# Kernel tuning notes

Hardware: AMD Instinct MI355X
Metric: run time of the kernel (lower is better)

Reference implementation:

```python
import math
import jax, jax.numpy as jnp
import numpy as np

D_MODEL = 1024
N_HEADS = 16
HEAD_DIM = D_MODEL // N_HEADS
D_FF = 4096
LN_EPS = 1e-5


def _layer_norm(x, g, b):
    mu = jnp.mean(x, axis=-1, keepdims=True)
    var = jnp.var(x, axis=-1, keepdims=True)
    return (x - mu) * jax.lax.rsqrt(var + LN_EPS) * g + b


def setup_inputs() -> dict:
    key = jax.random.key(0)
    ks = jax.random.split(key, 8)
    s = 0.02
    d, dff = D_MODEL, D_FF
    return {
        "src": jax.random.normal(ks[0], (2, 2048, d), dtype=jnp.float32),
        "in_proj_w": jax.random.normal(ks[1], (3 * d, d), dtype=jnp.float32) * s,
        "in_proj_b": jnp.zeros((3 * d,), dtype=jnp.float32),
        "out_w": jax.random.normal(ks[2], (d, d), dtype=jnp.float32) * s,
        "out_b": jnp.zeros((d,), dtype=jnp.float32),
        "lin1_w": jax.random.normal(ks[3], (dff, d), dtype=jnp.float32) * s,
        "lin1_b": jnp.zeros((dff,), dtype=jnp.float32),
        "lin2_w": jax.random.normal(ks[4], (d, dff), dtype=jnp.float32) * s,
        "lin2_b": jnp.zeros((d,), dtype=jnp.float32),
        "ln1_g": jnp.ones((d,), dtype=jnp.float32),
        "ln1_b": jnp.zeros((d,), dtype=jnp.float32),
        "ln2_g": jnp.ones((d,), dtype=jnp.float32),
        "ln2_b": jnp.zeros((d,), dtype=jnp.float32),
    }


def reference(src, in_proj_w, in_proj_b, out_w, out_b, lin1_w, lin1_b,
              lin2_w, lin2_b, ln1_g, ln1_b, ln2_g, ln2_b):
    B, S, d = src.shape
    # QKV projections (in_proj_weight split at d, then kv split)
    q = src @ in_proj_w[:d].T + in_proj_b[:d]              # [B,S,d]
    kv = src @ in_proj_w[d:].T + in_proj_b[d:]             # [B,S,2d]
    q = q.reshape(B, S, N_HEADS, HEAD_DIM)
    kv = kv.reshape(B, S, 2, N_HEADS, HEAD_DIM)
    k, v = kv[:, :, 0], kv[:, :, 1]
    softmax_scale = 1.0 / math.sqrt(HEAD_DIM)
    scores = jnp.einsum('bthd,bshd->bhts', q, k) * softmax_scale  # [B,H,Sq,Skv]
    # 'distribute': softmax over the QUERY dimension (dim=-2)
    attention = jax.nn.softmax(scores, axis=-2)
    post = jnp.einsum('bhts,bshd->bthd', attention, v)     # [B,Sq,H,hd]
    # post-attention activation 'gelu' (torch exact gelu)
    post = jax.nn.gelu(post, approximate=False)
    # attention_scale == 'sqrt': divide by sqrt(kv_len)
    post = post / math.sqrt(S)
    attn_out = post.reshape(B, S, d) @ out_w.T + out_b
    # post-norm residual structure (pre_norm=False, dropout=0)
    x = _layer_norm(src + attn_out, ln1_g, ln1_b)
    ff = jax.nn.gelu(x @ lin1_w.T + lin1_b, approximate=False) @ lin2_w.T + lin2_b
    return _layer_norm(x + ff, ln2_g, ln2_b)
```

## Files before the change

kernel.cpp:

```cpp
#include <hip/hip_runtime.h>
#include <hip/hip_bf16.h>
#include <math.h>


using bf16x8 = __attribute__((ext_vector_type(8))) short;
using f32x4  = __attribute__((ext_vector_type(4))) float;

__device__ inline f32x4 mfma16(bf16x8 a, bf16x8 b, f32x4 c) {
    return __builtin_amdgcn_mfma_f32_16x16x32_bf16(a, b, c, 0, 0, 0);
}

__device__ inline ushort f2bf(float f) {
    union { float f; unsigned u; } x; x.f = f;
    unsigned r = x.u + 0x7fffu + ((x.u >> 16) & 1u);
    return (ushort)(r >> 16);
}

__device__ inline float bf2f(ushort u) {
    union { unsigned u; float f; } x; x.u = ((unsigned)u) << 16; return x.f;
}

__device__ inline float gelu_exact(float v) {
    return 0.5f * v * (1.0f + erff(v * 0.70710678118654752f));
}

__device__ __forceinline__ void gl2lds16(const ushort* g, ushort* l) {
    __builtin_amdgcn_global_load_lds(
        (const __attribute__((address_space(1))) unsigned int*)g,
        (__attribute__((address_space(3))) unsigned int*)l,
        16, 0, 0);
}

__global__ __launch_bounds__(256) void cvt_kernel(const float4* __restrict__ in,
                                                  ushort* __restrict__ out, int n4) {
    int i = blockIdx.x * 256 + threadIdx.x;
    if (i >= n4) return;
    float4 v = in[i];
    ushort4 o;
    o.x = f2bf(v.x); o.y = f2bf(v.y); o.z = f2bf(v.z); o.w = f2bf(v.w);
    ((ushort4*)out)[i] = o;
}

__global__ __launch_bounds__(256) void gemm_bt(
    const ushort* __restrict__ A, const ushort* __restrict__ Bw,
    const float* __restrict__ bias, int M, int N, int K, int kLen, int mode,
    ushort* __restrict__ ob0, ushort* __restrict__ ob1, ushort* __restrict__ ob2,
    float* __restrict__ of) {
    __shared__ ushort As[128 * 32];
    __shared__ ushort Bs[128 * 32];
    int tid = threadIdx.x, lane = tid & 63, w = tid >> 6;
    int wm = w >> 1, wn = w & 1;
    int bm = blockIdx.y * 128, bn = blockIdx.x * 128;
    int kz = blockIdx.z;
    int q4 = lane >> 4, l15 = lane & 15;
    f32x4 acc[4][4] = {};

    int srow = w * 16 + (lane >> 2);
    int scg = lane & 3;
    const ushort* Ab = A + (size_t)bm * K + (size_t)kz * kLen;
    const ushort* Bb = Bw + (size_t)bn * K + (size_t)kz * kLen;
    const ushort* gA0 = Ab + (size_t)srow * K + scg * 8;
    const ushort* gA1 = Ab + (size_t)(64 + srow) * K + scg * 8;
    const ushort* gB0 = Bb + (size_t)srow * K + scg * 8;
    const ushort* gB1 = Bb + (size_t)(64 + srow) * K + scg * 8;
    ushort* lA0 = As + w * 512;
    ushort* lA1 = As + 2048 + w * 512;
    ushort* lB0 = Bs + w * 512;
    ushort* lB1 = Bs + 2048 + w * 512;

    const ushort* aP[4];
    const ushort* bP[4];
#pragma unroll
    for (int mi = 0; mi < 4; mi++)
        aP[mi] = As + (wm * 64 + mi * 16 + l15) * 32 + q4 * 8;
#pragma unroll
    for (int ni = 0; ni < 4; ni++)
        bP[ni] = Bs + (wn * 64 + ni * 16 + l15) * 32 + q4 * 8;

    for (int k0 = 0; k0 < kLen; k0 += 32) {
        __syncthreads();
        gl2lds16(gA0 + k0, lA0);
        gl2lds16(gA1 + k0, lA1);
        gl2lds16(gB0 + k0, lB0);
        gl2lds16(gB1 + k0, lB1);
        __syncthreads();
        bf16x8 af[4], bfr[4];
#pragma unroll
        for (int mi = 0; mi < 4; mi++) af[mi] = *(const bf16x8*)aP[mi];
#pragma unroll
        for (int ni = 0; ni < 4; ni++) bfr[ni] = *(const bf16x8*)bP[ni];
#pragma unroll
        for (int mi = 0; mi < 4; mi++)
#pragma unroll
            for (int ni = 0; ni < 4; ni++)
                acc[mi][ni] = mfma16(af[mi], bfr[ni], acc[mi][ni]);
    }

    int r0 = bm + wm * 64, c0 = bn + wn * 64;
#pragma unroll
    for (int mi = 0; mi < 4; mi++) {
#pragma unroll
        for (int ni = 0; ni < 4; ni++) {
            int colg = c0 + ni * 16 + l15;
            float bv = (mode == 3) ? 0.f : bias[colg];
#pragma unroll
            for (int r = 0; r < 4; r++) {
                int rowg = r0 + mi * 16 + q4 * 4 + r;
                float v = acc[mi][ni][r] + bv;
                if (mode == 0) {
                    if (colg < 1024) {
                        ob0[(size_t)rowg * 1024 + colg] = f2bf(v);
                    } else if (colg < 2048) {
                        ob1[(size_t)rowg * 1024 + (colg - 1024)] = f2bf(v);
                    } else {
                        int c = colg - 2048;
                        int hh = c >> 6, dh = c & 63;
                        int b = rowg >> 11, s = rowg & 2047;
                        ob2[((size_t)(b * 16 + hh) * 64 + dh) * 2048 + s] = f2bf(v);
                    }
                } else if (mode == 2) {
                    ob0[(size_t)rowg * N + colg] = f2bf(gelu_exact(v));
                } else {
                    of[(size_t)kz * M * N + (size_t)rowg * N + colg] = v;
                }
            }
        }
    }
}

__global__ __launch_bounds__(256) void attn_colsum(const ushort* __restrict__ qb,
                                                   const ushort* __restrict__ kb,
                                                   float* __restrict__ ninv) {
    __shared__ ushort Qs[64 * 72];
    int tid = threadIdx.x, lane = tid & 63, w = tid >> 6;
    int bh = blockIdx.x >> 4, sblk = blockIdx.x & 15;
    int b = bh >> 4, h = bh & 15;
    int q4 = lane >> 4, l15 = lane & 15;
    const ushort* qbase = qb + (size_t)(b * 2048) * 1024 + h * 64;
    const ushort* kbase = kb + (size_t)(b * 2048) * 1024 + h * 64;
    int s_base = sblk * 128 + w * 32;

    bf16x8 ka[2][2];
#pragma unroll
    for (int mi = 0; mi < 2; mi++) {
        const ushort* kp = kbase + (size_t)(s_base + mi * 16 + l15) * 1024 + q4 * 8;
        ka[mi][0] = *(const bf16x8*)(kp);
        ka[mi][1] = *(const bf16x8*)(kp + 32);
    }
    float acc[2][4] = {};

    int sr = tid >> 3;
    int sc = (tid & 7) * 8;
    for (int t0 = 0; t0 < 2048; t0 += 64) {
        uint4 g0 = *(const uint4*)(qbase + (size_t)(t0 + sr) * 1024 + sc);
        uint4 g1 = *(const uint4*)(qbase + (size_t)(t0 + 32 + sr) * 1024 + sc);
        __syncthreads();
        *(uint4*)&Qs[sr * 72 + sc] = g0;
        *(uint4*)&Qs[(32 + sr) * 72 + sc] = g1;
        __syncthreads();
#pragma unroll
        for (int tsub = 0; tsub < 4; tsub++) {
            bf16x8 bq0 = *(const bf16x8*)&Qs[(tsub * 16 + l15) * 72 + q4 * 8];
            bf16x8 bq1 = *(const bf16x8*)&Qs[(tsub * 16 + l15) * 72 + 32 + q4 * 8];
#pragma unroll
            for (int mi = 0; mi < 2; mi++) {
                f32x4 d = {0.f, 0.f, 0.f, 0.f};
                d = mfma16(ka[mi][0], bq0, d);
                d = mfma16(ka[mi][1], bq1, d);
#pragma unroll
                for (int r = 0; r < 4; r++)
                    acc[mi][r] += __expf(d[r] * 0.125f);
            }
        }
    }
#pragma unroll
    for (int mi = 0; mi < 2; mi++)
#pragma unroll
        for (int r = 0; r < 4; r++) {
            float v = acc[mi][r];
            v += __shfl_xor(v, 1); v += __shfl_xor(v, 2);
            v += __shfl_xor(v, 4); v += __shfl_xor(v, 8);
            if (l15 == 0)
                ninv[(size_t)bh * 2048 + s_base + mi * 16 + q4 * 4 + r] = 1.f / v;
        }
}

__global__ __launch_bounds__(256) void scale_vt(ushort* __restrict__ vt,
                                                const float* __restrict__ ninv) {
    int g = blockIdx.x * 256 + threadIdx.x;
    size_t base = (size_t)g * 8;
    int bh = g >> 14;
    int s = (int)(base & 2047);
    float4 n0 = ((const float4*)(ninv + (size_t)bh * 2048 + s))[0];
    float4 n1 = ((const float4*)(ninv + (size_t)bh * 2048 + s))[1];
    ushort4 a = ((const ushort4*)(vt + base))[0];
    ushort4 c = ((const ushort4*)(vt + base))[1];
    ushort4 oa, oc;
    oa.x = f2bf(bf2f(a.x) * n0.x); oa.y = f2bf(bf2f(a.y) * n0.y);
    oa.z = f2bf(bf2f(a.z) * n0.z); oa.w = f2bf(bf2f(a.w) * n0.w);
    oc.x = f2bf(bf2f(c.x) * n1.x); oc.y = f2bf(bf2f(c.y) * n1.y);
    oc.z = f2bf(bf2f(c.z) * n1.z); oc.w = f2bf(bf2f(c.w) * n1.w);
    ((ushort4*)(vt + base))[0] = oa;
    ((ushort4*)(vt + base))[1] = oc;
}

__global__ __launch_bounds__(256) void attn_pv(const ushort* __restrict__ qb,
                                               const ushort* __restrict__ kb,
                                               const ushort* __restrict__ vt,
                                               ushort* __restrict__ post) {
    __shared__ ushort Ks[64 * 72];
    __shared__ ushort Vs[64 * 72];
    __shared__ ushort Ps[4][32 * 72];
    int tid = threadIdx.x, lane = tid & 63, w = tid >> 6;
    int bh = blockIdx.x >> 4, tblk = blockIdx.x & 15;
    int b = bh >> 4, h = bh & 15;
    int q4 = lane >> 4, l15 = lane & 15;
    const ushort* qbase = qb + (size_t)(b * 2048) * 1024 + h * 64;
    const ushort* kbase = kb + (size_t)(b * 2048) * 1024 + h * 64;
    const ushort* vtb = vt + (size_t)bh * 64 * 2048;
    int t_base = tblk * 128 + w * 32;

    bf16x8 aq[2][2];
#pragma unroll
    for (int mi = 0; mi < 2; mi++) {
        const ushort* qp = qbase + (size_t)(t_base + mi * 16 + l15) * 1024 + q4 * 8;
        aq[mi][0] = *(const bf16x8*)(qp);
        aq[mi][1] = *(const bf16x8*)(qp + 32);
    }
    f32x4 oacc[2][4] = {};
    ushort* myP = Ps[w];

    int sr = tid >> 3;
    int sc = (tid & 7) * 8;
    for (int s0 = 0; s0 < 2048; s0 += 64) {
        uint4 k0g = *(const uint4*)(kbase + (size_t)(s0 + sr) * 1024 + sc);
        uint4 k1g = *(const uint4*)(kbase + (size_t)(s0 + 32 + sr) * 1024 + sc);
        uint4 v0g = *(const uint4*)(vtb + (size_t)sr * 2048 + s0 + sc);
        uint4 v1g = *(const uint4*)(vtb + (size_t)(32 + sr) * 2048 + s0 + sc);
        __syncthreads();
        *(uint4*)&Ks[sr * 72 + sc] = k0g;
        *(uint4*)&Ks[(32 + sr) * 72 + sc] = k1g;
        *(uint4*)&Vs[sr * 72 + sc] = v0g;
        *(uint4*)&Vs[(32 + sr) * 72 + sc] = v1g;
        __syncthreads();
#pragma unroll
        for (int ssub = 0; ssub < 4; ssub++) {
            bf16x8 bk0 = *(const bf16x8*)&Ks[(ssub * 16 + l15) * 72 + q4 * 8];
            bf16x8 bk1 = *(const bf16x8*)&Ks[(ssub * 16 + l15) * 72 + 32 + q4 * 8];
#pragma unroll
            for (int mi = 0; mi < 2; mi++) {
                f32x4 d = {0.f, 0.f, 0.f, 0.f};
                d = mfma16(aq[mi][0], bk0, d);
                d = mfma16(aq[mi][1], bk1, d);
#pragma unroll
                for (int r = 0; r < 4; r++)
                    myP[(mi * 16 + q4 * 4 + r) * 72 + ssub * 16 + l15] =
                        f2bf(__expf(d[r] * 0.125f));
            }
        }
        bf16x8 bv[4][2];
#pragma unroll
        for (int ni = 0; ni < 4; ni++) {
            bv[ni][0] = *(const bf16x8*)&Vs[(ni * 16 + l15) * 72 + q4 * 8];
            bv[ni][1] = *(const bf16x8*)&Vs[(ni * 16 + l15) * 72 + 32 + q4 * 8];
        }
#pragma unroll
        for (int mi = 0; mi < 2; mi++) {
            bf16x8 ap0 = *(const bf16x8*)&myP[(mi * 16 + l15) * 72 + q4 * 8];
            bf16x8 ap1 = *(const bf16x8*)&myP[(mi * 16 + l15) * 72 + 32 + q4 * 8];
#pragma unroll
            for (int ni = 0; ni < 4; ni++) {
                oacc[mi][ni] = mfma16(ap0, bv[ni][0], oacc[mi][ni]);
                oacc[mi][ni] = mfma16(ap1, bv[ni][1], oacc[mi][ni]);
            }
        }
    }
#pragma unroll
    for (int mi = 0; mi < 2; mi++)
#pragma unroll
        for (int ni = 0; ni < 4; ni++)
#pragma unroll
            for (int r = 0; r < 4; r++) {
                int t = t_base + mi * 16 + q4 * 4 + r;
                float g = gelu_exact(oacc[mi][ni][r]) * 0.022097086912079608f;
                post[(size_t)(b * 2048 + t) * 1024 + h * 64 + ni * 16 + l15] = f2bf(g);
            }
}

__global__ __launch_bounds__(256) void ln_comb(const float* __restrict__ p0,
                                               const float* __restrict__ p1,
                                               const float* __restrict__ bias,
                                               const float* __restrict__ res,
                                               const float* __restrict__ gw,
                                               const float* __restrict__ bw,
                                               ushort* __restrict__ outb,
                                               float* __restrict__ outf) {
    int row = blockIdx.x, tid = threadIdx.x;
    int lane = tid & 63, wid = tid >> 6;
    size_t off = (size_t)row * 1024;
    float4 a = ((const float4*)(p0 + off))[tid];
    float4 b = ((const float4*)(p1 + off))[tid];
    float4 r = ((const float4*)(res + off))[tid];
    float4 bb = ((const float4*)bias)[tid];
    float4 v;
    v.x = a.x + b.x + r.x + bb.x;
    v.y = a.y + b.y + r.y + bb.y;
    v.z = a.z + b.z + r.z + bb.z;
    v.w = a.w + b.w + r.w + bb.w;
    float s = v.x + v.y + v.z + v.w;
    float ss = v.x * v.x + v.y * v.y + v.z * v.z + v.w * v.w;
    for (int m = 1; m < 64; m <<= 1) { s += __shfl_xor(s, m); ss += __shfl_xor(ss, m); }
    __shared__ float red[8];
    if (lane == 0) { red[wid] = s; red[wid + 4] = ss; }
    __syncthreads();
    s = red[0] + red[1] + red[2] + red[3];
    ss = red[4] + red[5] + red[6] + red[7];
    float mu = s * (1.f / 1024.f);
    float var = ss * (1.f / 1024.f) - mu * mu;
    float inv = rsqrtf(var + 1e-5f);
    float4 gv = ((const float4*)gw)[tid];
    float4 bv = ((const float4*)bw)[tid];
    float o0 = (v.x - mu) * inv * gv.x + bv.x;
    float o1 = (v.y - mu) * inv * gv.y + bv.y;
    float o2 = (v.z - mu) * inv * gv.z + bv.z;
    float o3 = (v.w - mu) * inv * gv.w + bv.w;
    if (outf) {
        float4 o; o.x = o0; o.y = o1; o.z = o2; o.w = o3;
        ((float4*)(outf + off))[tid] = o;
    }
    if (outb) {
        ushort4 o; o.x = f2bf(o0); o.y = f2bf(o1); o.z = f2bf(o2); o.w = f2bf(o3);
        ((ushort4*)(outb + off))[tid] = o;
    }
}

extern "C" void kernel_launch(void* const* d_in, const int* in_sizes, int n_in,
                              void* d_out, int out_size, void* d_ws, size_t ws_size,
                              hipStream_t stream) {
    const float* src  = (const float*)d_in[0];
    const float* w_in = (const float*)d_in[1];
    const float* b_in = (const float*)d_in[2];
    const float* w_o  = (const float*)d_in[3];
    const float* b_o  = (const float*)d_in[4];
    const float* w1   = (const float*)d_in[5];
    const float* b1   = (const float*)d_in[6];
    const float* w2   = (const float*)d_in[7];
    const float* b2   = (const float*)d_in[8];
    const float* g1   = (const float*)d_in[9];
    const float* be1  = (const float*)d_in[10];
    const float* g2   = (const float*)d_in[11];
    const float* be2  = (const float*)d_in[12];
    float* out = (float*)d_out;

    const size_t M = 4096;
    char* wsp = (char*)d_ws;
    size_t off = 0;
    auto alloc = [&](size_t bytes) -> void* {
        void* p = wsp + off;
        off = (off + bytes + 255) & ~(size_t)255;
        return p;
    };
    ushort* src_bf  = (ushort*)alloc(M * 1024 * 2);
    ushort* win_bf  = (ushort*)alloc(3072 * 1024 * 2);
    ushort* wout_bf = (ushort*)alloc(1024 * 1024 * 2);
    ushort* w1_bf   = (ushort*)alloc(4096 * 1024 * 2);
    ushort* w2_bf   = (ushort*)alloc((size_t)1024 * 4096 * 2);
    ushort* q_bf    = (ushort*)alloc(M * 1024 * 2);
    ushort* k_bf    = (ushort*)alloc(M * 1024 * 2);
    ushort* vt_bf   = (ushort*)alloc(M * 1024 * 2);
    float*  ninv    = (float*)alloc(2 * 16 * 2048 * 4);
    ushort* post_bf = (ushort*)alloc(M * 1024 * 2);
    float*  part    = (float*)alloc(2 * M * 1024 * 4);
    ushort* x_bf    = (ushort*)alloc(M * 1024 * 2);
    float*  x_f32   = (float*)alloc(M * 1024 * 4);
    ushort* h1_bf   = (ushort*)alloc(M * 4096 * 2);

    cvt_kernel<<<4096, 256, 0, stream>>>((const float4*)src, src_bf, 1048576);
    cvt_kernel<<<3072, 256, 0, stream>>>((const float4*)w_in, win_bf, 786432);
    cvt_kernel<<<1024, 256, 0, stream>>>((const float4*)w_o, wout_bf, 262144);
    cvt_kernel<<<4096, 256, 0, stream>>>((const float4*)w1, w1_bf, 1048576);
    cvt_kernel<<<4096, 256, 0, stream>>>((const float4*)w2, w2_bf, 1048576);

    gemm_bt<<<dim3(24, 32, 1), 256, 0, stream>>>(src_bf, win_bf, b_in, 4096, 3072, 1024, 1024, 0,
                                                 q_bf, k_bf, vt_bf, nullptr);

    attn_colsum<<<512, 256, 0, stream>>>(q_bf, k_bf, ninv);
    scale_vt<<<2048, 256, 0, stream>>>(vt_bf, ninv);
    attn_pv<<<512, 256, 0, stream>>>(q_bf, k_bf, vt_bf, post_bf);

    gemm_bt<<<dim3(8, 32, 2), 256, 0, stream>>>(post_bf, wout_bf, b_o, 4096, 1024, 1024, 512, 3,
                                                nullptr, nullptr, nullptr, part);
    ln_comb<<<4096, 256, 0, stream>>>(part, part + M * 1024, b_o, src, g1, be1, x_bf, x_f32);

    gemm_bt<<<dim3(32, 32, 1), 256, 0, stream>>>(x_bf, w1_bf, b1, 4096, 4096, 1024, 1024, 2,
                                                 h1_bf, nullptr, nullptr, nullptr);
    gemm_bt<<<dim3(8, 32, 2), 256, 0, stream>>>(h1_bf, w2_bf, b2, 4096, 1024, 4096, 2048, 3,
                                                nullptr, nullptr, nullptr, part);
    ln_comb<<<4096, 256, 0, stream>>>(part, part + M * 1024, b2, x_f32, g2, be2, nullptr, out);
}
```

Baseline: 487.8 us.

## Merge conversions, use bf16 4-way split-K partials, transpose V separately, approximate GELU

Replaces the five fp32-to-bf16 conversion launches with one combined kernel. The split-K GEMMs go from 2 to 4 K-splits and write bf16 partials instead of fp32, and the LayerNorm kernel now sums four partial planes. The QKV GEMM stores V row-major, and a new LDS-tiled kernel scales and transposes it, replacing the strided transposed stores and the in-place scale pass. Exact erf GELU is swapped for a tanh-style exp approximation, which lowers accuracy, as do the bf16 partial sums.

```diff
diff --git a/kernel.cpp b/kernel.cpp
--- a/kernel.cpp
+++ b/kernel.cpp
@@ -20,8 +20,10 @@
     union { unsigned u; float f; } x; x.u = ((unsigned)u) << 16; return x.f;
 }
 
-__device__ inline float gelu_exact(float v) {
-    return 0.5f * v * (1.0f + erff(v * 0.70710678118654752f));
+__device__ inline float gelu_fast(float v) {
+    float u = v * (1.5957691216f + 0.0713548162f * v * v);
+    float e = __expf(u);
+    return v * (e / (e + 1.0f));
 }
 
 __device__ __forceinline__ void gl2lds16(const ushort* g, ushort* l) {
@@ -31,21 +33,30 @@
         16, 0, 0);
 }
 
-__global__ __launch_bounds__(256) void cvt_kernel(const float4* __restrict__ in,
-                                                  ushort* __restrict__ out, int n4) {
+__global__ __launch_bounds__(256) void cvt_all(const float4* __restrict__ s0,
+                                               const float4* __restrict__ s1,
+                                               const float4* __restrict__ s2,
+                                               const float4* __restrict__ s3,
+                                               const float4* __restrict__ s4,
+                                               ushort4* __restrict__ out) {
     int i = blockIdx.x * 256 + threadIdx.x;
-    if (i >= n4) return;
-    float4 v = in[i];
+    const float4* p;
+    int off;
+    if (i < 1048576)      { p = s0; off = i; }
+    else if (i < 1835008) { p = s1; off = i - 1048576; }
+    else if (i < 2097152) { p = s2; off = i - 1835008; }
+    else if (i < 3145728) { p = s3; off = i - 2097152; }
+    else                  { p = s4; off = i - 3145728; }
+    float4 v = p[off];
     ushort4 o;
     o.x = f2bf(v.x); o.y = f2bf(v.y); o.z = f2bf(v.z); o.w = f2bf(v.w);
-    ((ushort4*)out)[i] = o;
+    out[i] = o;
 }
 
 __global__ __launch_bounds__(256) void gemm_bt(
     const ushort* __restrict__ A, const ushort* __restrict__ Bw,
     const float* __restrict__ bias, int M, int N, int K, int kLen, int mode,
-    ushort* __restrict__ ob0, ushort* __restrict__ ob1, ushort* __restrict__ ob2,
-    float* __restrict__ of) {
+    ushort* __restrict__ ob0, ushort* __restrict__ ob1, ushort* __restrict__ ob2) {
     __shared__ ushort As[128 * 32];
     __shared__ ushort Bs[128 * 32];
     int tid = threadIdx.x, lane = tid & 63, w = tid >> 6;
@@ -113,15 +124,12 @@
                     } else if (colg < 2048) {
                         ob1[(size_t)rowg * 1024 + (colg - 1024)] = f2bf(v);
                     } else {
-                        int c = colg - 2048;
-                        int hh = c >> 6, dh = c & 63;
-                        int b = rowg >> 11, s = rowg & 2047;
-                        ob2[((size_t)(b * 16 + hh) * 64 + dh) * 2048 + s] = f2bf(v);
+                        ob2[(size_t)rowg * 1024 + (colg - 2048)] = f2bf(v);
                     }
                 } else if (mode == 2) {
-                    ob0[(size_t)rowg * N + colg] = f2bf(gelu_exact(v));
+                    ob0[(size_t)rowg * N + colg] = f2bf(gelu_fast(v));
                 } else {
-                    of[(size_t)kz * M * N + (size_t)rowg * N + colg] = v;
+                    ob0[(size_t)kz * M * N + (size_t)rowg * N + colg] = f2bf(v);
                 }
             }
         }
@@ -185,23 +193,40 @@
         }
 }
 
-__global__ __launch_bounds__(256) void scale_vt(ushort* __restrict__ vt,
-                                                const float* __restrict__ ninv) {
-    int g = blockIdx.x * 256 + threadIdx.x;
-    size_t base = (size_t)g * 8;
-    int bh = g >> 14;
-    int s = (int)(base & 2047);
-    float4 n0 = ((const float4*)(ninv + (size_t)bh * 2048 + s))[0];
-    float4 n1 = ((const float4*)(ninv + (size_t)bh * 2048 + s))[1];
-    ushort4 a = ((const ushort4*)(vt + base))[0];
-    ushort4 c = ((const ushort4*)(vt + base))[1];
-    ushort4 oa, oc;
-    oa.x = f2bf(bf2f(a.x) * n0.x); oa.y = f2bf(bf2f(a.y) * n0.y);
-    oa.z = f2bf(bf2f(a.z) * n0.z); oa.w = f2bf(bf2f(a.w) * n0.w);
-    oc.x = f2bf(bf2f(c.x) * n1.x); oc.y = f2bf(bf2f(c.y) * n1.y);
-    oc.z = f2bf(bf2f(c.z) * n1.z); oc.w = f2bf(bf2f(c.w) * n1.w);
-    ((ushort4*)(vt + base))[0] = oa;
-    ((ushort4*)(vt + base))[1] = oc;
+__global__ __launch_bounds__(256) void vt_scale_transpose(const ushort* __restrict__ vrow,
+                                                          const float* __restrict__ ninv,
+                                                          ushort* __restrict__ vt) {
+    __shared__ ushort T[64 * 72];
+    int tid = threadIdx.x;
+    int bh = blockIdx.x >> 5, sch = blockIdx.x & 31;
+    int b = bh >> 4, h = bh & 15;
+    int s0 = sch * 64;
+    int sl = tid >> 3, dh = (tid & 7) * 8;
+#pragma unroll
+    for (int rep = 0; rep < 2; rep++) {
+        int s = sl + rep * 32;
+        float n = ninv[(size_t)bh * 2048 + s0 + s];
+        const ushort* p = vrow + (size_t)(b * 2048 + s0 + s) * 1024 + h * 64 + dh;
+        ushort4 u0 = ((const ushort4*)p)[0];
+        ushort4 u1 = ((const ushort4*)p)[1];
+        ushort4 o0, o1;
+        o0.x = f2bf(bf2f(u0.x) * n); o0.y = f2bf(bf2f(u0.y) * n);
+        o0.z = f2bf(bf2f(u0.z) * n); o0.w = f2bf(bf2f(u0.w) * n);
+        o1.x = f2bf(bf2f(u1.x) * n); o1.y = f2bf(bf2f(u1.y) * n);
+        o1.z = f2bf(bf2f(u1.z) * n); o1.w = f2bf(bf2f(u1.w) * n);
+        *(ushort4*)&T[s * 72 + dh] = o0;
+        *(ushort4*)&T[s * 72 + dh + 4] = o1;
+    }
+    __syncthreads();
+    int dhl = tid >> 3, soff = (tid & 7) * 8;
+#pragma unroll
+    for (int rep = 0; rep < 2; rep++) {
+        int d = dhl + rep * 32;
+        ushort tmp[8];
+#pragma unroll
+        for (int j = 0; j < 8; j++) tmp[j] = T[(soff + j) * 72 + d];
+        *(uint4*)(vt + ((size_t)bh * 64 + d) * 2048 + s0 + soff) = *(uint4*)tmp;
+    }
 }
 
 __global__ __launch_bounds__(256) void attn_pv(const ushort* __restrict__ qb,
@@ -282,31 +307,31 @@
 #pragma unroll
             for (int r = 0; r < 4; r++) {
                 int t = t_base + mi * 16 + q4 * 4 + r;
-                float g = gelu_exact(oacc[mi][ni][r]) * 0.022097086912079608f;
+                float g = gelu_fast(oacc[mi][ni][r]) * 0.022097086912079608f;
                 post[(size_t)(b * 2048 + t) * 1024 + h * 64 + ni * 16 + l15] = f2bf(g);
             }
 }
 
-__global__ __launch_bounds__(256) void ln_comb(const float* __restrict__ p0,
-                                               const float* __restrict__ p1,
-                                               const float* __restrict__ bias,
-                                               const float* __restrict__ res,
-                                               const float* __restrict__ gw,
-                                               const float* __restrict__ bw,
-                                               ushort* __restrict__ outb,
-                                               float* __restrict__ outf) {
+__global__ __launch_bounds__(256) void ln_comb4(const ushort* __restrict__ parts,
+                                                const float* __restrict__ bias,
+                                                const float* __restrict__ res,
+                                                const float* __restrict__ gw,
+                                                const float* __restrict__ bw,
+                                                ushort* __restrict__ outb,
+                                                float* __restrict__ outf) {
+    const size_t PLANE = (size_t)4096 * 1024;
     int row = blockIdx.x, tid = threadIdx.x;
     int lane = tid & 63, wid = tid >> 6;
-    size_t off = (size_t)row * 1024;
-    float4 a = ((const float4*)(p0 + off))[tid];
-    float4 b = ((const float4*)(p1 + off))[tid];
-    float4 r = ((const float4*)(res + off))[tid];
-    float4 bb = ((const float4*)bias)[tid];
+    size_t off = (size_t)row * 1024 + tid * 4;
+    float4 r = *(const float4*)(res + off);
+    float4 bb = *(const float4*)(bias + tid * 4);
     float4 v;
-    v.x = a.x + b.x + r.x + bb.x;
-    v.y = a.y + b.y + r.y + bb.y;
-    v.z = a.z + b.z + r.z + bb.z;
-    v.w = a.w + b.w + r.w + bb.w;
+    v.x = r.x + bb.x; v.y = r.y + bb.y; v.z = r.z + bb.z; v.w = r.w + bb.w;
+#pragma unroll
+    for (int p = 0; p < 4; p++) {
+        ushort4 u = *(const ushort4*)(parts + p * PLANE + off);
+        v.x += bf2f(u.x); v.y += bf2f(u.y); v.z += bf2f(u.z); v.w += bf2f(u.w);
+    }
     float s = v.x + v.y + v.z + v.w;
     float ss = v.x * v.x + v.y * v.y + v.z * v.z + v.w * v.w;
     for (int m = 1; m < 64; m <<= 1) { s += __shfl_xor(s, m); ss += __shfl_xor(ss, m); }
@@ -318,19 +343,19 @@
     float mu = s * (1.f / 1024.f);
     float var = ss * (1.f / 1024.f) - mu * mu;
     float inv = rsqrtf(var + 1e-5f);
-    float4 gv = ((const float4*)gw)[tid];
-    float4 bv = ((const float4*)bw)[tid];
+    float4 gv = *(const float4*)(gw + tid * 4);
+    float4 bv = *(const float4*)(bw + tid * 4);
     float o0 = (v.x - mu) * inv * gv.x + bv.x;
     float o1 = (v.y - mu) * inv * gv.y + bv.y;
     float o2 = (v.z - mu) * inv * gv.z + bv.z;
     float o3 = (v.w - mu) * inv * gv.w + bv.w;
     if (outf) {
         float4 o; o.x = o0; o.y = o1; o.z = o2; o.w = o3;
-        ((float4*)(outf + off))[tid] = o;
+        *(float4*)(outf + off) = o;
     }
     if (outb) {
         ushort4 o; o.x = f2bf(o0); o.y = f2bf(o1); o.z = f2bf(o2); o.w = f2bf(o3);
-        ((ushort4*)(outb + off))[tid] = o;
+        *(ushort4*)(outb + off) = o;
     }
 }
 
@@ -370,31 +395,30 @@
     ushort* vt_bf   = (ushort*)alloc(M * 1024 * 2);
     float*  ninv    = (float*)alloc(2 * 16 * 2048 * 4);
     ushort* post_bf = (ushort*)alloc(M * 1024 * 2);
-    float*  part    = (float*)alloc(2 * M * 1024 * 4);
+    ushort* part    = (ushort*)alloc(4 * M * 1024 * 2);
     ushort* x_bf    = (ushort*)alloc(M * 1024 * 2);
     float*  x_f32   = (float*)alloc(M * 1024 * 4);
     ushort* h1_bf   = (ushort*)alloc(M * 4096 * 2);
-
-    cvt_kernel<<<4096, 256, 0, stream>>>((const float4*)src, src_bf, 1048576);
-    cvt_kernel<<<3072, 256, 0, stream>>>((const float4*)w_in, win_bf, 786432);
-    cvt_kernel<<<1024, 256, 0, stream>>>((const float4*)w_o, wout_bf, 262144);
-    cvt_kernel<<<4096, 256, 0, stream>>>((const float4*)w1, w1_bf, 1048576);
-    cvt_kernel<<<4096, 256, 0, stream>>>((const float4*)w2, w2_bf, 1048576);
+    ushort* v_row   = part;
+
+    cvt_all<<<16384, 256, 0, stream>>>((const float4*)src, (const float4*)w_in,
+                                       (const float4*)w_o, (const float4*)w1,
+                                       (const float4*)w2, (ushort4*)src_bf);
 
     gemm_bt<<<dim3(24, 32, 1), 256, 0, stream>>>(src_bf, win_bf, b_in, 4096, 3072, 1024, 1024, 0,
-                                                 q_bf, k_bf, vt_bf, nullptr);
+                                                 q_bf, k_bf, v_row);
 
     attn_colsum<<<512, 256, 0, stream>>>(q_bf, k_bf, ninv);
-    scale_vt<<<2048, 256, 0, stream>>>(vt_bf, ninv);
+    vt_scale_transpose<<<1024, 256, 0, stream>>>(v_row, ninv, vt_bf);
     attn_pv<<<512, 256, 0, stream>>>(q_bf, k_bf, vt_bf, post_bf);
 
-    gemm_bt<<<dim3(8, 32, 2), 256, 0, stream>>>(post_bf, wout_bf, b_o, 4096, 1024, 1024, 512, 3,
-                                                nullptr, nullptr, nullptr, part);
-    ln_comb<<<4096, 256, 0, stream>>>(part, part + M * 1024, b_o, src, g1, be1, x_bf, x_f32);
+    gemm_bt<<<dim3(8, 32, 4), 256, 0, stream>>>(post_bf, wout_bf, b_o, 4096, 1024, 1024, 256, 3,
+                                                part, nullptr, nullptr);
+    ln_comb4<<<4096, 256, 0, stream>>>(part, b_o, src, g1, be1, x_bf, x_f32);
 
     gemm_bt<<<dim3(32, 32, 1), 256, 0, stream>>>(x_bf, w1_bf, b1, 4096, 4096, 1024, 1024, 2,
-                                                 h1_bf, nullptr, nullptr, nullptr);
-    gemm_bt<<<dim3(8, 32, 2), 256, 0, stream>>>(h1_bf, w2_bf, b2, 4096, 1024, 4096, 2048, 3,
-                                                nullptr, nullptr, nullptr, part);
-    ln_comb<<<4096, 256, 0, stream>>>(part, part + M * 1024, b2, x_f32, g2, be2, nullptr, out);
-}
+                                                 h1_bf, nullptr, nullptr);
+    gemm_bt<<<dim3(8, 32, 4), 256, 0, stream>>>(h1_bf, w2_bf, b2, 4096, 1024, 4096, 1024, 3,
+                                                part, nullptr, nullptr);
+    ln_comb4<<<4096, 256, 0, stream>>>(part, b2, x_f32, g2, be2, nullptr, out);
+}
```

Measured after the change: 484.8 us. Within noise of the previous version (-0.6%).
